# Kernel tuning notes

Hardware: AMD Instinct MI355X
Metric: run time of the kernel (lower is better)

The kernel has to match this reference:

```python
import jax, jax.numpy as jnp
import numpy as np

N = 40000
IN_DIM = 128
HID = 64
E = 640000


def sage_conv(x, edge_index, W_l, b_l, W_r):
    """PyG SAGEConv with mean aggregation.
    out = lin_l(mean_{j in N(i)} x_j) + lin_r(x_i)
    edge_index[0]=src (message source), edge_index[1]=dst (aggregation target).
    """
    src, dst = edge_index[0], edge_index[1]
    n = x.shape[0]
    msgs = x[src]                                            # [E, d] gather
    sums = jax.ops.segment_sum(msgs, dst, num_segments=n)    # [N, d]
    cnt = jax.ops.segment_sum(jnp.ones((msgs.shape[0],), x.dtype), dst,
                              num_segments=n)                # [N]
    mean = sums / jnp.maximum(cnt, 1.0)[:, None]
    return mean @ W_l.T + b_l + x @ W_r.T


def setup_inputs() -> dict:
    key = jax.random.key(0)
    ks = jax.random.split(key, 8)
    x = jax.random.normal(ks[0], (N, IN_DIM), dtype=jnp.float32)
    edge_index = jax.random.randint(ks[1], (2, E), 0, N, dtype=jnp.int32)
    s1 = 1.0 / np.sqrt(IN_DIM)
    s2 = 1.0 / np.sqrt(HID)
    W1_l = jax.random.uniform(ks[2], (HID, IN_DIM), jnp.float32, -s1, s1)
    b1_l = jax.random.uniform(ks[3], (HID,), jnp.float32, -s1, s1)
    W1_r = jax.random.uniform(ks[4], (HID, IN_DIM), jnp.float32, -s1, s1)
    W2_l = jax.random.uniform(ks[5], (HID, HID), jnp.float32, -s2, s2)
    b2_l = jax.random.uniform(ks[6], (HID,), jnp.float32, -s2, s2)
    W2_r = jax.random.uniform(ks[7], (HID, HID), jnp.float32, -s2, s2)
    return {"x": x, "edge_index": edge_index,
            "W1_l": W1_l, "b1_l": b1_l, "W1_r": W1_r,
            "W2_l": W2_l, "b2_l": b2_l, "W2_r": W2_r}


def reference(x, edge_index, W1_l, b1_l, W1_r, W2_l, b2_l, W2_r):
    h = sage_conv(x, edge_index, W1_l, b1_l, W1_r)
    h = jax.nn.relu(h)
    # dropout is identity in eval mode (reference baseline is deterministic)
    z = sage_conv(h, edge_index, W2_l, b2_l, W2_r)
    return z
```

## Files before the change

### kernel.cpp

```cpp
#include <hip/hip_runtime.h>

#define INDIM 128
#define HID 64
#define CAP 64
#define GEMM_BLOCKS 625
#define SCAT_BLOCKS 1875

__device__ __forceinline__ float bf2f(unsigned short u) {
    union { unsigned int i; float f; } c; c.i = ((unsigned int)u) << 16; return c.f;
}
__device__ __forceinline__ unsigned short f2bf(float f) {
    union { float f; unsigned int i; } c; c.f = f;
    return (unsigned short)((c.i + 0x7FFFu + ((c.i >> 16) & 1u)) >> 16);
}

__device__ __forceinline__ float4 gather4(const unsigned short* __restrict__ Pb,
                                          int row, int f4) {
    const uint2 v = *(const uint2*)&Pb[(size_t)row * 64 + f4 * 4];
    float4 r;
    r.x = bf2f((unsigned short)(v.x & 0xffffu));
    r.y = bf2f((unsigned short)(v.x >> 16));
    r.z = bf2f((unsigned short)(v.y & 0xffffu));
    r.w = bf2f((unsigned short)(v.y >> 16));
    return r;
}

__device__ __forceinline__ float4 agg_core(const unsigned short* __restrict__ Pb,
                                           int idx0, int deg, int q, int f4) {
    float4 acc = make_float4(0.f, 0.f, 0.f, 0.f);
    const int nchunk = (deg + 3) >> 2;
    for (int c = 0; c < nchunk; c += 4) {
        #pragma unroll
        for (int u = 0; u < 4; ++u) {
            const int cc = c + u;
            const int lanesel = cc * 4 + q;
            const int sidx = __shfl(idx0, lanesel, 64);
            const float m = (cc < nchunk && lanesel < deg) ? 1.f : 0.f;
            const float4 v = gather4(Pb, sidx, f4);
            acc.x += v.x * m; acc.y += v.y * m;
            acc.z += v.z * m; acc.w += v.w * m;
        }
    }
    acc.x += __shfl_xor(acc.x, 16, 64); acc.y += __shfl_xor(acc.y, 16, 64);
    acc.z += __shfl_xor(acc.z, 16, 64); acc.w += __shfl_xor(acc.w, 16, 64);
    acc.x += __shfl_xor(acc.x, 32, 64); acc.y += __shfl_xor(acc.y, 32, 64);
    acc.z += __shfl_xor(acc.z, 32, 64); acc.w += __shfl_xor(acc.w, 32, 64);
    return acc;
}


__global__ __launch_bounds__(256) void k_prep(
    const float* __restrict__ W1l, const float* __restrict__ W1r,
    const float* __restrict__ W2l, const float* __restrict__ W2r,
    float* __restrict__ WT1l, float* __restrict__ WT1r,
    float* __restrict__ WT2l, float* __restrict__ WT2r,
    int* __restrict__ cnt, int n) {
    int gtid = blockIdx.x * 256 + threadIdx.x;
    if (gtid < n) cnt[gtid] = 0;
    if (gtid < 64 * 128) {
        int j = gtid >> 7, k = gtid & 127;
        WT1l[k * 64 + j] = W1l[gtid];
        WT1r[k * 64 + j] = W1r[gtid];
    }
    if (gtid < 64 * 64) {
        int j = gtid >> 6, k = gtid & 63;
        WT2l[k * 64 + j] = W2l[gtid];
        WT2r[k * 64 + j] = W2r[gtid];
    }
}


__global__ __launch_bounds__(256) void k_gemm1_scatter(
    const float* __restrict__ A,
    const float* __restrict__ WTl, const float* __restrict__ WTr,
    unsigned short* __restrict__ Pb, float* __restrict__ Q,
    const int* __restrict__ src, const int* __restrict__ dst,
    int* __restrict__ cnt, unsigned short* __restrict__ sorted, int N, int E) {
    __shared__ float As[64][INDIM + 1];
    const int tid = threadIdx.x;

    if (blockIdx.x >= GEMM_BLOCKS) {
        const int b = blockIdx.x - GEMM_BLOCKS;
        const int stride = SCAT_BLOCKS * 256;
        for (int e = b * 256 + tid; e < E; e += stride) {
            const int d = dst[e];
            const int slot = atomicAdd(&cnt[d], 1);
            if (slot < CAP) sorted[(d << 6) + slot] = (unsigned short)src[e];
        }
        return;
    }

    const int bm = blockIdx.x * 64;
    for (int idx = tid; idx < 64 * 32; idx += 256) {
        int row = idx >> 5, kq = idx & 31;
        const float4 v = ((const float4*)A)[(size_t)(bm + row) * 32 + kq];
        As[row][kq * 4 + 0] = v.x; As[row][kq * 4 + 1] = v.y;
        As[row][kq * 4 + 2] = v.z; As[row][kq * 4 + 3] = v.w;
    }
    __syncthreads();

    const int tx = tid & 15, ty = tid >> 4;
    const int n0 = ty * 4;
    float accl[4][4] = {}, accr[4][4] = {};
    #pragma unroll 8
    for (int k = 0; k < INDIM; ++k) {
        float a[4];
        #pragma unroll
        for (int i = 0; i < 4; ++i) a[i] = As[n0 + i][k];
        const float4 blv = ((const float4*)WTl)[k * 16 + tx];
        const float4 brv = ((const float4*)WTr)[k * 16 + tx];
        const float bl[4] = {blv.x, blv.y, blv.z, blv.w};
        const float br[4] = {brv.x, brv.y, brv.z, brv.w};
        #pragma unroll
        for (int i = 0; i < 4; ++i) {
            #pragma unroll
            for (int j = 0; j < 4; ++j) {
                accl[i][j] += a[i] * bl[j];
                accr[i][j] += a[i] * br[j];
            }
        }
    }
    #pragma unroll
    for (int i = 0; i < 4; ++i) {
        int m = bm + n0 + i;
        ushort4 pv;
        pv.x = f2bf(accl[i][0]); pv.y = f2bf(accl[i][1]);
        pv.z = f2bf(accl[i][2]); pv.w = f2bf(accl[i][3]);
        ((ushort4*)Pb)[(size_t)m * 16 + tx] = pv;
        ((float4*)Q)[(size_t)m * 16 + tx] =
            make_float4(accr[i][0], accr[i][1], accr[i][2], accr[i][3]);
    }
}


__global__ __launch_bounds__(512) void k_agg1_gemm2(
    const unsigned short* __restrict__ Pb, const float* __restrict__ Q,
    const float* __restrict__ b1,
    const int* __restrict__ cnt, const unsigned short* __restrict__ sorted,
    const float* __restrict__ WTl, const float* __restrict__ WTr,
    unsigned short* __restrict__ Pb2, float* __restrict__ Q2, int N) {
    __shared__ float Hs[64][HID + 4];
    const int tid = threadIdx.x;
    const int bm = blockIdx.x * 64;
    const int lane = tid & 63, w = tid >> 6;
    const int q = lane >> 4, f4 = lane & 15;
    const float4 bv4 = *(const float4*)&b1[f4 * 4];
    const int node_base = bm + w * 8;

    int degv = (lane < 8 && node_base + lane < N) ? cnt[node_base + lane] : 0;
    int degs[8], idx0s[8];
    #pragma unroll
    for (int r = 0; r < 8; ++r) {
        int d = __shfl(degv, r, 64);
        d = (d > CAP) ? CAP : d;
        degs[r] = d;
        const int ls = (lane < d) ? lane : ((d > 0) ? d - 1 : 0);
        idx0s[r] = (d > 0) ? (int)sorted[((node_base + r) << 6) + ls] : 0;
    }

    #pragma unroll
    for (int r = 0; r < 8; ++r) {
        const int node = node_base + r;
        if (node >= N) break;
        const float4 a = agg_core(Pb, idx0s[r], degs[r], q, f4);
        if (q == 0) {
            const float inv = 1.0f / fmaxf((float)degs[r], 1.0f);
            const float4 qv = *(const float4*)&Q[(size_t)node * 64 + f4 * 4];
            float4 hv;
            hv.x = fmaxf(a.x * inv + bv4.x + qv.x, 0.f);
            hv.y = fmaxf(a.y * inv + bv4.y + qv.y, 0.f);
            hv.z = fmaxf(a.z * inv + bv4.z + qv.z, 0.f);
            hv.w = fmaxf(a.w * inv + bv4.w + qv.w, 0.f);
            *(float4*)&Hs[w * 8 + r][f4 * 4] = hv;
        }
    }
    __syncthreads();

    const int tx = tid & 15, ty = tid >> 4;
    const int n0 = ty * 2;
    float accl[2][4] = {}, accr[2][4] = {};
    #pragma unroll 8
    for (int k = 0; k < HID; ++k) {
        float a[2];
        #pragma unroll
        for (int i = 0; i < 2; ++i) a[i] = Hs[n0 + i][k];
        const float4 blv = ((const float4*)WTl)[k * 16 + tx];
        const float4 brv = ((const float4*)WTr)[k * 16 + tx];
        const float bl[4] = {blv.x, blv.y, blv.z, blv.w};
        const float br[4] = {brv.x, brv.y, brv.z, brv.w};
        #pragma unroll
        for (int i = 0; i < 2; ++i) {
            #pragma unroll
            for (int j = 0; j < 4; ++j) {
                accl[i][j] += a[i] * bl[j];
                accr[i][j] += a[i] * br[j];
            }
        }
    }
    #pragma unroll
    for (int i = 0; i < 2; ++i) {
        int m = bm + n0 + i;
        if (m < N) {
            ushort4 pv;
            pv.x = f2bf(accl[i][0]); pv.y = f2bf(accl[i][1]);
            pv.z = f2bf(accl[i][2]); pv.w = f2bf(accl[i][3]);
            ((ushort4*)Pb2)[(size_t)m * 16 + tx] = pv;
            ((float4*)Q2)[(size_t)m * 16 + tx] =
                make_float4(accr[i][0], accr[i][1], accr[i][2], accr[i][3]);
        }
    }
}


__global__ __launch_bounds__(256) void k_agg2(
    const unsigned short* __restrict__ Pb2, const float* __restrict__ Q2,
    const float* __restrict__ b2,
    const int* __restrict__ cnt, const unsigned short* __restrict__ sorted,
    float* __restrict__ z, int N) {
    const int wid  = (blockIdx.x * 256 + threadIdx.x) >> 6;
    const int lane = threadIdx.x & 63;
    const int q = lane >> 4, f4 = lane & 15;
    if (wid >= N) return;
    int deg = cnt[wid]; if (deg > CAP) deg = CAP;
    const int ls = (lane < deg) ? lane : ((deg > 0) ? deg - 1 : 0);
    const int idx0 = (deg > 0) ? (int)sorted[(wid << 6) + ls] : 0;
    const float4 a = agg_core(Pb2, idx0, deg, q, f4);
    if (q == 0) {
        const float inv = 1.0f / fmaxf((float)deg, 1.0f);
        const float4 qv = *(const float4*)&Q2[(size_t)wid * 64 + f4 * 4];
        const float4 bv = *(const float4*)&b2[f4 * 4];
        float4 zv;
        zv.x = a.x * inv + bv.x + qv.x;
        zv.y = a.y * inv + bv.y + qv.y;
        zv.z = a.z * inv + bv.z + qv.z;
        zv.w = a.w * inv + bv.w + qv.w;
        *(float4*)&z[(size_t)wid * 64 + f4 * 4] = zv;
    }
}


extern "C" void kernel_launch(void* const* d_in, const int* in_sizes, int n_in,
                              void* d_out, int out_size, void* d_ws, size_t ws_size,
                              hipStream_t stream) {
    const float* x   = (const float*)d_in[0];
    const int*  edge = (const int*)d_in[1];
    const float* W1l = (const float*)d_in[2];
    const float* b1l = (const float*)d_in[3];
    const float* W1r = (const float*)d_in[4];
    const float* W2l = (const float*)d_in[5];
    const float* b2l = (const float*)d_in[6];
    const float* W2r = (const float*)d_in[7];

    const int N = in_sizes[0] / INDIM;
    const int E = in_sizes[1] / 2;
    const int* src = edge;
    const int* dst = edge + E;

    char* w = (char*)d_ws;
    auto carve = [&](size_t bytes) {
        char* p = w; w += (bytes + 255) & ~(size_t)255; return p;
    };
    unsigned short* Pb  = (unsigned short*)carve((size_t)N * 64 * 2);
    unsigned short* Pb2 = (unsigned short*)carve((size_t)N * 64 * 2);
    float* Q    = (float*)carve((size_t)N * 64 * 4);
    float* Q2   = (float*)carve((size_t)N * 64 * 4);
    float* WT1l = (float*)carve(128 * 64 * 4);
    float* WT1r = (float*)carve(128 * 64 * 4);
    float* WT2l = (float*)carve(64 * 64 * 4);
    float* WT2r = (float*)carve(64 * 64 * 4);
    int* cnt    = (int*)carve((size_t)N * 4);
    unsigned short* sorted = (unsigned short*)carve((size_t)N * CAP * 2);

    float* zout = (float*)d_out;

    const int gT = (N + 63) / 64;
    const int gN = (N + 255) / 256;

    k_prep<<<gN, 256, 0, stream>>>(W1l, W1r, W2l, W2r,
                                   WT1l, WT1r, WT2l, WT2r, cnt, N);
    k_gemm1_scatter<<<GEMM_BLOCKS + SCAT_BLOCKS, 256, 0, stream>>>(
        x, WT1l, WT1r, Pb, Q, src, dst, cnt, sorted, N, E);
    k_agg1_gemm2<<<gT, 512, 0, stream>>>(Pb, Q, b1l, cnt, sorted,
                                         WT2l, WT2r, Pb2, Q2, N);
    k_agg2<<<(N * 64 + 255) / 256, 256, 0, stream>>>(Pb2, Q2, b2l, cnt, sorted,
                                                     zout, N);
}
```

Measured before the change: 106.3 us.

## Pad degree counters and split fused layer-1 aggregation from layer-2 GEMM

Each per-node degree counter now sits on its own 128-byte stride, which is meant to cut atomic contention and cache-line sharing between neighbouring counters during the scatter. The fused aggregate-then-GEMM kernel is split into a one-wave-per-node aggregation kernel that writes H to global memory, followed by a separate tiled GEMM kernel with 4x4 register tiles. The Pb and Q buffers are reused for the layer-2 outputs. In exchange, H makes an extra round trip through global memory, an extra kernel launch is added, and the counter array grows 32x.

```diff
diff --git a/kernel.cpp b/kernel.cpp
--- a/kernel.cpp
+++ b/kernel.cpp
@@ -5,6 +5,7 @@
 #define CAP 64
 #define GEMM_BLOCKS 625
 #define SCAT_BLOCKS 1875
+#define CNTS 5
 
 __device__ __forceinline__ float bf2f(unsigned short u) {
     union { unsigned int i; float f; } c; c.i = ((unsigned int)u) << 16; return c.f;
@@ -56,7 +57,7 @@
     float* __restrict__ WT2l, float* __restrict__ WT2r,
     int* __restrict__ cnt, int n) {
     int gtid = blockIdx.x * 256 + threadIdx.x;
-    if (gtid < n) cnt[gtid] = 0;
+    if (gtid < n) cnt[gtid << CNTS] = 0;
     if (gtid < 64 * 128) {
         int j = gtid >> 7, k = gtid & 127;
         WT1l[k * 64 + j] = W1l[gtid];
@@ -84,7 +85,7 @@
         const int stride = SCAT_BLOCKS * 256;
         for (int e = b * 256 + tid; e < E; e += stride) {
             const int d = dst[e];
-            const int slot = atomicAdd(&cnt[d], 1);
+            const int slot = atomicAdd(&cnt[d << CNTS], 1);
             if (slot < CAP) sorted[(d << 6) + slot] = (unsigned short)src[e];
         }
         return;
@@ -133,63 +134,62 @@
 }
 
 
-__global__ __launch_bounds__(512) void k_agg1_gemm2(
+__global__ __launch_bounds__(256) void k_agg1(
     const unsigned short* __restrict__ Pb, const float* __restrict__ Q,
     const float* __restrict__ b1,
     const int* __restrict__ cnt, const unsigned short* __restrict__ sorted,
+    float* __restrict__ H, int N) {
+    const int wid  = (blockIdx.x * 256 + threadIdx.x) >> 6;
+    const int lane = threadIdx.x & 63;
+    const int q = lane >> 4, f4 = lane & 15;
+    if (wid >= N) return;
+    int deg = cnt[wid << CNTS]; if (deg > CAP) deg = CAP;
+    const int ls = (lane < deg) ? lane : ((deg > 0) ? deg - 1 : 0);
+    const int idx0 = (deg > 0) ? (int)sorted[(wid << 6) + ls] : 0;
+    const float4 a = agg_core(Pb, idx0, deg, q, f4);
+    if (q == 0) {
+        const float inv = 1.0f / fmaxf((float)deg, 1.0f);
+        const float4 qv = *(const float4*)&Q[(size_t)wid * 64 + f4 * 4];
+        const float4 bv = *(const float4*)&b1[f4 * 4];
+        float4 hv;
+        hv.x = fmaxf(a.x * inv + bv.x + qv.x, 0.f);
+        hv.y = fmaxf(a.y * inv + bv.y + qv.y, 0.f);
+        hv.z = fmaxf(a.z * inv + bv.z + qv.z, 0.f);
+        hv.w = fmaxf(a.w * inv + bv.w + qv.w, 0.f);
+        *(float4*)&H[(size_t)wid * 64 + f4 * 4] = hv;
+    }
+}
+
+
+__global__ __launch_bounds__(256) void k_gemm2(
+    const float* __restrict__ H,
     const float* __restrict__ WTl, const float* __restrict__ WTr,
     unsigned short* __restrict__ Pb2, float* __restrict__ Q2, int N) {
-    __shared__ float Hs[64][HID + 4];
+    __shared__ float As[64][HID + 1];
     const int tid = threadIdx.x;
     const int bm = blockIdx.x * 64;
-    const int lane = tid & 63, w = tid >> 6;
-    const int q = lane >> 4, f4 = lane & 15;
-    const float4 bv4 = *(const float4*)&b1[f4 * 4];
-    const int node_base = bm + w * 8;
-
-    int degv = (lane < 8 && node_base + lane < N) ? cnt[node_base + lane] : 0;
-    int degs[8], idx0s[8];
-    #pragma unroll
-    for (int r = 0; r < 8; ++r) {
-        int d = __shfl(degv, r, 64);
-        d = (d > CAP) ? CAP : d;
-        degs[r] = d;
-        const int ls = (lane < d) ? lane : ((d > 0) ? d - 1 : 0);
-        idx0s[r] = (d > 0) ? (int)sorted[((node_base + r) << 6) + ls] : 0;
-    }
-
-    #pragma unroll
-    for (int r = 0; r < 8; ++r) {
-        const int node = node_base + r;
-        if (node >= N) break;
-        const float4 a = agg_core(Pb, idx0s[r], degs[r], q, f4);
-        if (q == 0) {
-            const float inv = 1.0f / fmaxf((float)degs[r], 1.0f);
-            const float4 qv = *(const float4*)&Q[(size_t)node * 64 + f4 * 4];
-            float4 hv;
-            hv.x = fmaxf(a.x * inv + bv4.x + qv.x, 0.f);
-            hv.y = fmaxf(a.y * inv + bv4.y + qv.y, 0.f);
-            hv.z = fmaxf(a.z * inv + bv4.z + qv.z, 0.f);
-            hv.w = fmaxf(a.w * inv + bv4.w + qv.w, 0.f);
-            *(float4*)&Hs[w * 8 + r][f4 * 4] = hv;
-        }
+    for (int idx = tid; idx < 64 * 16; idx += 256) {
+        int row = idx >> 4, kq = idx & 15;
+        const float4 v = ((const float4*)H)[(size_t)(bm + row) * 16 + kq];
+        As[row][kq * 4 + 0] = v.x; As[row][kq * 4 + 1] = v.y;
+        As[row][kq * 4 + 2] = v.z; As[row][kq * 4 + 3] = v.w;
     }
     __syncthreads();
 
     const int tx = tid & 15, ty = tid >> 4;
-    const int n0 = ty * 2;
-    float accl[2][4] = {}, accr[2][4] = {};
+    const int n0 = ty * 4;
+    float accl[4][4] = {}, accr[4][4] = {};
     #pragma unroll 8
     for (int k = 0; k < HID; ++k) {
-        float a[2];
-        #pragma unroll
-        for (int i = 0; i < 2; ++i) a[i] = Hs[n0 + i][k];
+        float a[4];
+        #pragma unroll
+        for (int i = 0; i < 4; ++i) a[i] = As[n0 + i][k];
         const float4 blv = ((const float4*)WTl)[k * 16 + tx];
         const float4 brv = ((const float4*)WTr)[k * 16 + tx];
         const float bl[4] = {blv.x, blv.y, blv.z, blv.w};
         const float br[4] = {brv.x, brv.y, brv.z, brv.w};
         #pragma unroll
-        for (int i = 0; i < 2; ++i) {
+        for (int i = 0; i < 4; ++i) {
             #pragma unroll
             for (int j = 0; j < 4; ++j) {
                 accl[i][j] += a[i] * bl[j];
@@ -198,7 +198,7 @@
         }
     }
     #pragma unroll
-    for (int i = 0; i < 2; ++i) {
+    for (int i = 0; i < 4; ++i) {
         int m = bm + n0 + i;
         if (m < N) {
             ushort4 pv;
@@ -221,7 +221,7 @@
     const int lane = threadIdx.x & 63;
     const int q = lane >> 4, f4 = lane & 15;
     if (wid >= N) return;
-    int deg = cnt[wid]; if (deg > CAP) deg = CAP;
+    int deg = cnt[wid << CNTS]; if (deg > CAP) deg = CAP;
     const int ls = (lane < deg) ? lane : ((deg > 0) ? deg - 1 : 0);
     const int idx0 = (deg > 0) ? (int)sorted[(wid << 6) + ls] : 0;
     const float4 a = agg_core(Pb2, idx0, deg, q, f4);
@@ -261,27 +261,26 @@
         char* p = w; w += (bytes + 255) & ~(size_t)255; return p;
     };
     unsigned short* Pb  = (unsigned short*)carve((size_t)N * 64 * 2);
-    unsigned short* Pb2 = (unsigned short*)carve((size_t)N * 64 * 2);
     float* Q    = (float*)carve((size_t)N * 64 * 4);
-    float* Q2   = (float*)carve((size_t)N * 64 * 4);
+    float* H    = (float*)carve((size_t)N * 64 * 4);
     float* WT1l = (float*)carve(128 * 64 * 4);
     float* WT1r = (float*)carve(128 * 64 * 4);
     float* WT2l = (float*)carve(64 * 64 * 4);
     float* WT2r = (float*)carve(64 * 64 * 4);
-    int* cnt    = (int*)carve((size_t)N * 4);
+    int* cnt    = (int*)carve((size_t)N * (4 << CNTS));
     unsigned short* sorted = (unsigned short*)carve((size_t)N * CAP * 2);
 
     float* zout = (float*)d_out;
 
     const int gT = (N + 63) / 64;
     const int gN = (N + 255) / 256;
+    const int gW = (N * 64 + 255) / 256;
 
     k_prep<<<gN, 256, 0, stream>>>(W1l, W1r, W2l, W2r,
                                    WT1l, WT1r, WT2l, WT2r, cnt, N);
     k_gemm1_scatter<<<GEMM_BLOCKS + SCAT_BLOCKS, 256, 0, stream>>>(
         x, WT1l, WT1r, Pb, Q, src, dst, cnt, sorted, N, E);
-    k_agg1_gemm2<<<gT, 512, 0, stream>>>(Pb, Q, b1l, cnt, sorted,
-                                         WT2l, WT2r, Pb2, Q2, N);
-    k_agg2<<<(N * 64 + 255) / 256, 256, 0, stream>>>(Pb2, Q2, b2l, cnt, sorted,
-                                                     zout, N);
-}
+    k_agg1<<<gW, 256, 0, stream>>>(Pb, Q, b1l, cnt, sorted, H, N);
+    k_gemm2<<<gT, 256, 0, stream>>>(H, WT2l, WT2r, Pb, Q, N);
+    k_agg2<<<gW, 256, 0, stream>>>(Pb, Q, b2l, cnt, sorted, zout, N);
+}
```

After: 118.4 us. 11.5% more time.
